# Kernel optimization log

Measured on AMD Instinct MI355X. Metric: run time of the kernel, lower is better.

The kernel has to match this reference:

```python
import jax, jax.numpy as jnp
import numpy as np

CHAN = 128
IN_CHAN = 3
NB_OUT = 10
K = 2  # maxPoolKer


def affine_grid(theta, H, W):
    # theta: [C,2,3] -> grid [C,H,W,2], torch F.affine_grid align_corners=False
    xs = (2.0 * jnp.arange(W, dtype=jnp.float32) + 1.0) / W - 1.0
    ys = (2.0 * jnp.arange(H, dtype=jnp.float32) + 1.0) / H - 1.0
    gx, gy = jnp.meshgrid(xs, ys)  # [H,W]
    base = jnp.stack([gx, gy, jnp.ones_like(gx)], axis=-1)  # [H,W,3]
    return jnp.einsum('crk,hwk->chwr', theta, base)  # [...,0]=x, [...,1]=y


def grid_sample(img, grid):
    # img [M,H,W], grid [M,H,W,2]; bilinear, zeros padding, align_corners=False
    M, H, W = img.shape
    ix = ((grid[..., 0] + 1.0) * W - 1.0) * 0.5
    iy = ((grid[..., 1] + 1.0) * H - 1.0) * 0.5
    x0 = jnp.floor(ix)
    y0 = jnp.floor(iy)
    wx = ix - x0
    wy = iy - y0

    def tap(xi, yi):
        valid = (xi >= 0) & (xi <= W - 1) & (yi >= 0) & (yi <= H - 1)
        xc = jnp.clip(xi, 0, W - 1).astype(jnp.int32)
        yc = jnp.clip(yi, 0, H - 1).astype(jnp.int32)
        v = jax.vmap(lambda im, y, x: im[y, x])(img, yc, xc)
        return jnp.where(valid, v, 0.0)

    v00 = tap(x0, y0)
    v01 = tap(x0 + 1.0, y0)
    v10 = tap(x0, y0 + 1.0)
    v11 = tap(x0 + 1.0, y0 + 1.0)
    return (1.0 - wy) * ((1.0 - wx) * v00 + wx * v01) + wy * ((1.0 - wx) * v10 + wx * v11)


def geom_layer(x, geo, lin, box):
    # x [B,Ci,H,W]; lin [C,Ci]; geo,box [C,2,3]
    B, Ci, H, W = x.shape
    C = lin.shape[0]
    y = jnp.einsum('ci,bihw->bchw', lin, x)  # channel linear combine
    grid = affine_grid(geo, H, W)            # [C,H,W,2], shared across batch
    samp = jax.vmap(lambda yb: grid_sample(yb, grid))(y)  # [B,C,H,W]
    bgrid = affine_grid(box, H, W)
    boxm = grid_sample(jnp.ones((C, H, W), samp.dtype), bgrid)  # BoxPool mask
    return samp * boxm[None]


def maxpool_g(x, k):
    # MaxPool2d_G: depthwise box-filter conv -> argmax -> gather window from padded x
    B, C, H, W = x.shape
    ch, cw = H // k, W // k
    ker = jnp.ones((1, 1, ch, cw), x.dtype) / (ch + cw)
    xr = x.reshape(B * C, 1, H, W)
    conv = jax.lax.conv_general_dilated(
        xr, ker, (1, 1), [(ch // 2, ch // 2), (cw // 2, cw // 2)])
    conv = conv[:, :, :H, :W].reshape(B, C, H * W)
    argm = jnp.argmax(conv, axis=-1)
    r = argm // H  # original code uses origImgSize[0]; assumes square H==W
    c = argm % W
    padH, padW = H + H // k, W + W // k
    top = padH // 2 - H // 2
    left = padW // 2 - W // 2
    padded = jnp.zeros((B, C, padH, padW), x.dtype).at[:, :, top:top + H, left:left + W].set(x)
    r2 = r + H // (2 * k)
    c2 = c + W // (2 * k)
    ri = r2[..., None] + (jnp.arange(ch) - ch // 2)  # [B,C,ch]
    ci = c2[..., None] + (jnp.arange(cw) - cw // 2)  # [B,C,cw]
    gat = jax.vmap(jax.vmap(lambda p, rr, cc: p[rr[:, None], cc[None, :]]))(padded, ri, ci)
    return gat  # [B,C,ch,cw]


def setup_inputs() -> dict:
    key = jax.random.key(0)
    ks = jax.random.split(key, 12)
    eye = jnp.eye(3, dtype=jnp.float32)[:2]  # [2,3]
    x = jax.random.normal(ks[0], (8, IN_CHAN, 64, 64), dtype=jnp.float32)
    geo0 = eye[None] + 0.1 * jax.random.normal(ks[1], (CHAN, 2, 3), dtype=jnp.float32)
    lin0 = jax.random.uniform(ks[2], (CHAN, IN_CHAN), dtype=jnp.float32)
    box0 = eye[None] + 0.1 * jax.random.normal(ks[3], (CHAN, 2, 3), dtype=jnp.float32)
    geos = eye[None, None] + 0.1 * jax.random.normal(ks[4], (3, CHAN, 2, 3), dtype=jnp.float32)
    lins = jax.random.uniform(ks[5], (3, CHAN, CHAN), dtype=jnp.float32)
    boxes = eye[None, None] + 0.1 * jax.random.normal(ks[6], (3, CHAN, 2, 3), dtype=jnp.float32)
    bound = 1.0 / np.sqrt(CHAN)
    dense_w = jax.random.uniform(ks[7], (NB_OUT, CHAN), dtype=jnp.float32, minval=-bound, maxval=bound)
    dense_b = jax.random.uniform(ks[8], (NB_OUT,), dtype=jnp.float32, minval=-bound, maxval=bound)
    return {"x": x, "geo0": geo0, "lin0": lin0, "box0": box0,
            "geos": geos, "lins": lins, "boxes": boxes,
            "dense_w": dense_w, "dense_b": dense_b}


def reference(x, geo0, lin0, box0, geos, lins, boxes, dense_w, dense_b):
    h = geom_layer(x, geo0, lin0, box0)            # inLay: [8,128,64,64]
    h = geom_layer(h, geos[0], lins[0], boxes[0])  # layer 0
    h = maxpool_g(h, K)                            # layer 1 (maxPoolPos=1): [8,128,32,32]
    h = geom_layer(h, geos[1], lins[1], boxes[1])  # layer 2
    h = geom_layer(h, geos[2], lins[2], boxes[2])  # layer 3
    feat = h
    pooled = feat.mean(axis=-1).mean(axis=-1)      # [B,C]
    out = pooled @ dense_w.T + dense_b             # [B,nbOut]
    return out, feat
```

## Files before the change

kernel.cpp:

```cpp
#include <hip/hip_runtime.h>

#define BB 8
#define CC 128

__global__ __launch_bounds__(256) void inlay_sample_kernel(
    const float* __restrict__ x, const float* __restrict__ lin,
    const float* __restrict__ geo, const float* __restrict__ box,
    const float* __restrict__ db, float* __restrict__ out,
    float* __restrict__ head) {
  const int H = 64, W = 64, HW = 4096;
  __shared__ __align__(16) float cp[64 * 68];
  int bc = blockIdx.x;
  int b = bc & 7;
  int c = bc >> 3;
  int tid = threadIdx.x;
  if (bc == 0 && tid < 80) head[tid] = db[tid % 10];
  const float* xb = x + (size_t)b * 3 * HW;

  float w0 = lin[c * 3 + 0], w1 = lin[c * 3 + 1], w2 = lin[c * 3 + 2];

#pragma unroll
  for (int k = 0; k < 4; ++k) {
    int i4 = tid + k * 256;
    int base = i4 * 4;
    float4 f0 = *reinterpret_cast<const float4*>(&xb[base]);
    float4 f1 = *reinterpret_cast<const float4*>(&xb[HW + base]);
    float4 f2 = *reinterpret_cast<const float4*>(&xb[2 * HW + base]);
    float4 cv;
    cv.x = w0 * f0.x + w1 * f1.x + w2 * f2.x;
    cv.y = w0 * f0.y + w1 * f1.y + w2 * f2.y;
    cv.z = w0 * f0.z + w1 * f1.z + w2 * f2.z;
    cv.w = w0 * f0.w + w1 * f1.w + w2 * f2.w;
    int h = i4 >> 4, w = (i4 & 15) * 4;
    *reinterpret_cast<float4*>(&cp[h * 68 + w]) = cv;
  }
  __syncthreads();

  const float* g = geo + c * 6;
  const float* bx = box + c * 6;
  float g0 = g[0], g1 = g[1], g2 = g[2], g3 = g[3], g4 = g[4], g5 = g[5];
  float b0 = bx[0], b1 = bx[1], b2 = bx[2], b3 = bx[3], b4 = bx[4], b5 = bx[5];
  float* o = out + ((size_t)b * CC + c) * HW;

#pragma unroll
  for (int k = 0; k < 16; ++k) {
    int px = tid + k * 256;
    int h = px >> 6, w = px & 63;
    float xs = (2.0f * w + 1.0f) / W - 1.0f;
    float ys = (2.0f * h + 1.0f) / H - 1.0f;
    float gx = g0 * xs + g1 * ys + g2;
    float gy = g3 * xs + g4 * ys + g5;
    float ix = ((gx + 1.0f) * W - 1.0f) * 0.5f;
    float iy = ((gy + 1.0f) * H - 1.0f) * 0.5f;
    float x0 = floorf(ix), y0 = floorf(iy);
    float wx = ix - x0, wy = iy - y0;
    float v[2][2];
#pragma unroll
    for (int dy = 0; dy < 2; ++dy)
#pragma unroll
      for (int dx = 0; dx < 2; ++dx) {
        float xf = x0 + dx, yf = y0 + dy;
        bool valid = (xf >= 0.0f) && (xf <= 63.0f) && (yf >= 0.0f) && (yf <= 63.0f);
        int xi = (int)fminf(fmaxf(xf, 0.0f), 63.0f);
        int yi = (int)fminf(fmaxf(yf, 0.0f), 63.0f);
        v[dy][dx] = valid ? cp[yi * 68 + xi] : 0.0f;
      }
    float samp = (1.0f - wy) * ((1.0f - wx) * v[0][0] + wx * v[0][1]) +
                 wy * ((1.0f - wx) * v[1][0] + wx * v[1][1]);

    float bgx = b0 * xs + b1 * ys + b2;
    float bgy = b3 * xs + b4 * ys + b5;
    float bix = ((bgx + 1.0f) * W - 1.0f) * 0.5f;
    float biy = ((bgy + 1.0f) * H - 1.0f) * 0.5f;
    float bx0 = floorf(bix), by0 = floorf(biy);
    float bwx = bix - bx0, bwy = biy - by0;
    float m[2][2];
#pragma unroll
    for (int dy = 0; dy < 2; ++dy)
#pragma unroll
      for (int dx = 0; dx < 2; ++dx) {
        float xf = bx0 + dx, yf = by0 + dy;
        m[dy][dx] = ((xf >= 0.0f) && (xf <= 63.0f) && (yf >= 0.0f) && (yf <= 63.0f)) ? 1.0f : 0.0f;
      }
    float mask = (1.0f - bwy) * ((1.0f - bwx) * m[0][0] + bwx * m[0][1]) +
                 bwy * ((1.0f - bwx) * m[1][0] + bwx * m[1][1]);
    o[px] = samp * mask;
  }
}

__global__ __launch_bounds__(256) void gemm64_kernel(
    const float* __restrict__ lin, const float* __restrict__ x,
    float* __restrict__ y, int HW) {
  const int Ci = 128;
  __shared__ __align__(16) float As[16][68];
  __shared__ __align__(16) float Bs[16][64];
  int bx = blockIdx.x;
  int b = bx & 7;
  int t = bx >> 3;
  int row0 = (t & 1) * 64;
  int col0 = (t >> 1) * 64;
  const float* xb = x + (size_t)b * Ci * HW;
  float* yb = y + (size_t)b * CC * HW;
  int tid = threadIdx.x;
  int tx = tid & 15, ty = tid >> 4;
  int m = tid >> 2, kq = (tid & 3) * 4;
  int kk = tid >> 4, n4 = (tid & 15) * 4;
  float acc[4][4] = {};
  float4 ra = *reinterpret_cast<const float4*>(&lin[(row0 + m) * Ci + kq]);
  float4 rb = *reinterpret_cast<const float4*>(&xb[(size_t)kk * HW + col0 + n4]);
  for (int k0 = 0; k0 < 128; k0 += 16) {
    __syncthreads();
    As[kq + 0][m] = ra.x; As[kq + 1][m] = ra.y; As[kq + 2][m] = ra.z; As[kq + 3][m] = ra.w;
    *reinterpret_cast<float4*>(&Bs[kk][n4]) = rb;
    __syncthreads();
    if (k0 + 16 < 128) {
      ra = *reinterpret_cast<const float4*>(&lin[(row0 + m) * Ci + k0 + 16 + kq]);
      rb = *reinterpret_cast<const float4*>(&xb[(size_t)(k0 + 16 + kk) * HW + col0 + n4]);
    }
#pragma unroll
    for (int kki = 0; kki < 16; ++kki) {
      float4 a4 = *reinterpret_cast<const float4*>(&As[kki][ty * 4]);
      float4 b4 = *reinterpret_cast<const float4*>(&Bs[kki][tx * 4]);
      float a[4] = {a4.x, a4.y, a4.z, a4.w};
      float bv[4] = {b4.x, b4.y, b4.z, b4.w};
#pragma unroll
      for (int i = 0; i < 4; i++)
#pragma unroll
        for (int j = 0; j < 4; j++) acc[i][j] += a[i] * bv[j];
    }
  }
#pragma unroll
  for (int i = 0; i < 4; i++) {
    float* yr = yb + (size_t)(row0 + ty * 4 + i) * HW + col0 + tx * 4;
    *reinterpret_cast<float4*>(yr) = make_float4(acc[i][0], acc[i][1], acc[i][2], acc[i][3]);
  }
}

__global__ __launch_bounds__(1024, 4) void sampmax_kernel(
    const float* __restrict__ y, const float* __restrict__ geo,
    const float* __restrict__ box, float* __restrict__ out) {
  __shared__ __align__(16) float sp[64 * 68];
  __shared__ __align__(16) float arena[64 * 100];
  __shared__ float wv[16];
  __shared__ int wi[16];
  __shared__ int am_s;
  float* pl = arena;
  float* cb = arena;

  int bc = blockIdx.x;
  int b = bc & 7;
  int c = bc >> 3;
  int tid = threadIdx.x;

  const float* plane = y + ((size_t)b * CC + c) * 4096;
  *reinterpret_cast<float4*>(&pl[tid * 4]) = *reinterpret_cast<const float4*>(&plane[tid * 4]);
  __syncthreads();

  {
    const float* g = geo + c * 6;
    const float* bx = box + c * 6;
    float g0 = g[0], g1 = g[1], g2 = g[2], g3 = g[3], g4 = g[4], g5 = g[5];
    float b0 = bx[0], b1 = bx[1], b2 = bx[2], b3 = bx[3], b4 = bx[4], b5 = bx[5];
#pragma unroll
    for (int k = 0; k < 4; ++k) {
      int px = tid + k * 1024;
      int h = px >> 6, w = px & 63;
      float xs = (2.0f * w + 1.0f) / 64.0f - 1.0f;
      float ys = (2.0f * h + 1.0f) / 64.0f - 1.0f;
      float gx = g0 * xs + g1 * ys + g2;
      float gy = g3 * xs + g4 * ys + g5;
      float ix = ((gx + 1.0f) * 64.0f - 1.0f) * 0.5f;
      float iy = ((gy + 1.0f) * 64.0f - 1.0f) * 0.5f;
      float x0 = floorf(ix), y0 = floorf(iy);
      float wx = ix - x0, wy = iy - y0;
      float v[2][2];
#pragma unroll
      for (int dy = 0; dy < 2; ++dy)
#pragma unroll
        for (int dx = 0; dx < 2; ++dx) {
          float xf = x0 + dx, yf = y0 + dy;
          bool valid = (xf >= 0.0f) && (xf <= 63.0f) && (yf >= 0.0f) && (yf <= 63.0f);
          int xi = (int)fminf(fmaxf(xf, 0.0f), 63.0f);
          int yi = (int)fminf(fmaxf(yf, 0.0f), 63.0f);
          v[dy][dx] = valid ? pl[yi * 64 + xi] : 0.0f;
        }
      float samp = (1.0f - wy) * ((1.0f - wx) * v[0][0] + wx * v[0][1]) +
                   wy * ((1.0f - wx) * v[1][0] + wx * v[1][1]);
      float bgx = b0 * xs + b1 * ys + b2;
      float bgy = b3 * xs + b4 * ys + b5;
      float bix = ((bgx + 1.0f) * 64.0f - 1.0f) * 0.5f;
      float biy = ((bgy + 1.0f) * 64.0f - 1.0f) * 0.5f;
      float bx0 = floorf(bix), by0 = floorf(biy);
      float bwx = bix - bx0, bwy = biy - by0;
      float m[2][2];
#pragma unroll
      for (int dy = 0; dy < 2; ++dy)
#pragma unroll
        for (int dx = 0; dx < 2; ++dx) {
          float xf = bx0 + dx, yf = by0 + dy;
          m[dy][dx] = ((xf >= 0.0f) && (xf <= 63.0f) && (yf >= 0.0f) && (yf <= 63.0f)) ? 1.0f : 0.0f;
        }
      float mask = (1.0f - bwy) * ((1.0f - bwx) * m[0][0] + bwx * m[0][1]) +
                   bwy * ((1.0f - bwx) * m[1][0] + bwx * m[1][1]);
      sp[h * 68 + w] = samp * mask;
    }
  }
  __syncthreads();

  if (tid < 256) {
    int strip = tid >> 4, w4 = (tid & 15) * 4;
    int h0 = strip * 4;
    float4 a = make_float4(0.f, 0.f, 0.f, 0.f);
    float4 keep0 = a, keep1 = a, keep2 = a;
#pragma unroll
    for (int j = 0; j < 32; ++j) {
      int r = h0 + j - 16;
      bool valid = (r >= 0) && (r < 64);
      int rc = valid ? r : 0;
      float4 f = *reinterpret_cast<const float4*>(&sp[rc * 68 + w4]);
      f.x = valid ? f.x : 0.0f; f.y = valid ? f.y : 0.0f;
      f.z = valid ? f.z : 0.0f; f.w = valid ? f.w : 0.0f;
      if (j == 0) keep0 = f;
      if (j == 1) keep1 = f;
      if (j == 2) keep2 = f;
      a.x += f.x; a.y += f.y; a.z += f.z; a.w += f.w;
    }
    *reinterpret_cast<float4*>(&cb[(h0 + 0) * 100 + 16 + w4]) = a;
#pragma unroll
    for (int j = 32; j < 35; ++j) {
      int r = h0 + j - 16;
      bool valid = (r < 64);
      int rc = valid ? r : 0;
      float4 f = *reinterpret_cast<const float4*>(&sp[rc * 68 + w4]);
      f.x = valid ? f.x : 0.0f; f.y = valid ? f.y : 0.0f;
      f.z = valid ? f.z : 0.0f; f.w = valid ? f.w : 0.0f;
      float4 kp = (j == 32) ? keep0 : ((j == 33) ? keep1 : keep2);
      a.x += f.x - kp.x; a.y += f.y - kp.y; a.z += f.z - kp.z; a.w += f.w - kp.w;
      *reinterpret_cast<float4*>(&cb[(h0 + j - 31) * 100 + 16 + w4]) = a;
    }
  } else if (tid < 768) {
    int l = tid - 256;
    int row = l >> 3, gq = l & 7;
    int base = row * 100 + ((gq < 4) ? gq * 4 : 80 + (gq - 4) * 4);
    *reinterpret_cast<float4*>(&cb[base]) = make_float4(0.f, 0.f, 0.f, 0.f);
  }
  __syncthreads();

  float best = -3.402823466e+38f;
  int bidx = 0x7fffffff;
  {
    int h = tid >> 4, w4 = (tid & 15) * 4;
    float s0 = 0.f, k0 = 0.f, k1 = 0.f, k2 = 0.f;
#pragma unroll
    for (int q = 0; q < 8; ++q) {
      float4 f = *reinterpret_cast<const float4*>(&cb[h * 100 + w4 + 4 * q]);
      if (q == 0) { k0 = f.x; k1 = f.y; k2 = f.z; }
      s0 += f.x; s0 += f.y; s0 += f.z; s0 += f.w;
    }
    float4 ft = *reinterpret_cast<const float4*>(&cb[h * 100 + w4 + 32]);
    float s1 = s0 - k0 + ft.x;
    float s2 = s1 - k1 + ft.y;
    float s3 = s2 - k2 + ft.z;
    float sv[4] = {s0, s1, s2, s3};
#pragma unroll
    for (int d = 0; d < 4; ++d) {
      int i = (h << 6) + w4 + d;
      if (sv[d] > best) { best = sv[d]; bidx = i; }
    }
  }
#pragma unroll
  for (int off = 32; off > 0; off >>= 1) {
    float v2 = __shfl_down(best, off);
    int i2 = __shfl_down(bidx, off);
    if (v2 > best || (v2 == best && i2 < bidx)) { best = v2; bidx = i2; }
  }
  if ((tid & 63) == 0) { wv[tid >> 6] = best; wi[tid >> 6] = bidx; }
  __syncthreads();
  if (tid == 0) {
    float bv = wv[0]; int bi = wi[0];
#pragma unroll
    for (int k = 1; k < 16; ++k)
      if (wv[k] > bv || (wv[k] == bv && wi[k] < bi)) { bv = wv[k]; bi = wi[k]; }
    am_s = bi;
  }
  __syncthreads();

  int am = am_s;
  int r = am >> 6, cx = am & 63;
  float* o = out + ((size_t)b * CC + c) * 1024;
  {
    int oi = tid >> 5, oj = tid & 31;
    int rr = r + oi - 16, cj = cx + oj - 16;
    bool v = (rr >= 0) && (rr < 64) && (cj >= 0) && (cj < 64);
    int rrc = v ? rr : 0, cjc = v ? cj : 0;
    o[tid] = v ? sp[rrc * 68 + cjc] : 0.0f;
  }
}

template <bool POOL>
__global__ __launch_bounds__(512) void fused32_kernel(
    const float* __restrict__ lin, const float* __restrict__ x,
    const float* __restrict__ geo, const float* __restrict__ box,
    float* __restrict__ out, const float* __restrict__ dw,
    float* __restrict__ head) {
  const int H = 32, W = 32, HW = 1024;
  __shared__ __align__(16) float pls[4][1024];
  __shared__ float wred[32];
  __shared__ float wsum[4];
  int b = blockIdx.x & 7;
  int c0 = (blockIdx.x >> 3) * 4;
  int tid = threadIdx.x;
  const float* xb = x + (size_t)b * 128 * HW;
  const float* l0 = lin + (c0 + 0) * 128;
  const float* l1 = lin + (c0 + 1) * 128;
  const float* l2 = lin + (c0 + 2) * 128;
  const float* l3 = lin + (c0 + 3) * 128;
  int px2 = tid * 2;

  float2 a0 = make_float2(0.f, 0.f), a1 = a0, a2 = a0, a3 = a0;
#pragma unroll 8
  for (int k = 0; k < 128; ++k) {
    float2 xv = *reinterpret_cast<const float2*>(&xb[(size_t)k * HW + px2]);
    float s0 = l0[k], s1 = l1[k], s2 = l2[k], s3 = l3[k];
    a0.x += s0 * xv.x; a0.y += s0 * xv.y;
    a1.x += s1 * xv.x; a1.y += s1 * xv.y;
    a2.x += s2 * xv.x; a2.y += s2 * xv.y;
    a3.x += s3 * xv.x; a3.y += s3 * xv.y;
  }
  *reinterpret_cast<float2*>(&pls[0][px2]) = a0;
  *reinterpret_cast<float2*>(&pls[1][px2]) = a1;
  *reinterpret_cast<float2*>(&pls[2][px2]) = a2;
  *reinterpret_cast<float2*>(&pls[3][px2]) = a3;
  __syncthreads();

  float psum[4] = {0.f, 0.f, 0.f, 0.f};
#pragma unroll
  for (int c = 0; c < 4; ++c) {
    const float* g = geo + (c0 + c) * 6;
    const float* bxp = box + (c0 + c) * 6;
    float g0 = g[0], g1 = g[1], g2 = g[2], g3 = g[3], g4 = g[4], g5 = g[5];
    float b0 = bxp[0], b1 = bxp[1], b2 = bxp[2], b3 = bxp[3], b4 = bxp[4], b5 = bxp[5];
    float* o = out + ((size_t)b * CC + c0 + c) * HW;
    const float* pl = pls[c];
#pragma unroll
    for (int k = 0; k < 2; ++k) {
      int px = tid + k * 512;
      int h = px >> 5, w = px & 31;
      float xs = (2.0f * w + 1.0f) / W - 1.0f;
      float ys = (2.0f * h + 1.0f) / H - 1.0f;
      float gx = g0 * xs + g1 * ys + g2;
      float gy = g3 * xs + g4 * ys + g5;
      float ix = ((gx + 1.0f) * W - 1.0f) * 0.5f;
      float iy = ((gy + 1.0f) * H - 1.0f) * 0.5f;
      float x0 = floorf(ix), y0 = floorf(iy);
      float wx = ix - x0, wy = iy - y0;
      float v[2][2];
#pragma unroll
      for (int dy = 0; dy < 2; ++dy)
#pragma unroll
        for (int dx = 0; dx < 2; ++dx) {
          float xf = x0 + dx, yf = y0 + dy;
          bool valid = (xf >= 0.0f) && (xf <= 31.0f) && (yf >= 0.0f) && (yf <= 31.0f);
          int xi = (int)fminf(fmaxf(xf, 0.0f), 31.0f);
          int yi = (int)fminf(fmaxf(yf, 0.0f), 31.0f);
          v[dy][dx] = valid ? pl[yi * 32 + xi] : 0.0f;
        }
      float samp = (1.0f - wy) * ((1.0f - wx) * v[0][0] + wx * v[0][1]) +
                   wy * ((1.0f - wx) * v[1][0] + wx * v[1][1]);
      float bgx = b0 * xs + b1 * ys + b2;
      float bgy = b3 * xs + b4 * ys + b5;
      float bix = ((bgx + 1.0f) * W - 1.0f) * 0.5f;
      float biy = ((bgy + 1.0f) * H - 1.0f) * 0.5f;
      float bx0 = floorf(bix), by0 = floorf(biy);
      float bwx = bix - bx0, bwy = biy - by0;
      float m[2][2];
#pragma unroll
      for (int dy = 0; dy < 2; ++dy)
#pragma unroll
        for (int dx = 0; dx < 2; ++dx) {
          float xf = bx0 + dx, yf = by0 + dy;
          m[dy][dx] = ((xf >= 0.0f) && (xf <= 31.0f) && (yf >= 0.0f) && (yf <= 31.0f)) ? 1.0f : 0.0f;
        }
      float mask = (1.0f - bwy) * ((1.0f - bwx) * m[0][0] + bwx * m[0][1]) +
                   bwy * ((1.0f - bwx) * m[1][0] + bwx * m[1][1]);
      float res = samp * mask;
      o[px] = res;
      if (POOL) psum[c] += res;
    }
  }
  if (POOL) {
    int lane = tid & 63, wid = tid >> 6;
#pragma unroll
    for (int c = 0; c < 4; ++c) {
      float r = psum[c];
#pragma unroll
      for (int off = 32; off > 0; off >>= 1) r += __shfl_down(r, off);
      if (lane == 0) wred[c * 8 + wid] = r;
    }
    __syncthreads();
    if (tid < 4) {
      float t = 0.f;
#pragma unroll
      for (int w = 0; w < 8; ++w) t += wred[tid * 8 + w];
      wsum[tid] = t * (1.0f / 1024.0f);
    }
    __syncthreads();
    if (tid < 10) {
      float s = 0.f;
#pragma unroll
      for (int c = 0; c < 4; ++c) s += wsum[c] * dw[tid * 128 + c0 + c];
      atomicAdd(&head[b * 10 + tid], s);
    }
  }
}

extern "C" void kernel_launch(void* const* d_in, const int* in_sizes, int n_in,
                              void* d_out, int out_size, void* d_ws, size_t ws_size,
                              hipStream_t stream) {
  const float* x     = (const float*)d_in[0];
  const float* geo0  = (const float*)d_in[1];
  const float* lin0  = (const float*)d_in[2];
  const float* box0  = (const float*)d_in[3];
  const float* geos  = (const float*)d_in[4];
  const float* lins  = (const float*)d_in[5];
  const float* boxes = (const float*)d_in[6];
  const float* dw    = (const float*)d_in[7];
  const float* db    = (const float*)d_in[8];

  float* out  = (float*)d_out;
  float* feat = out + 80;
  float* ws   = (float*)d_ws;
  float* ws0  = ws;
  float* ws1  = ws + 4194304;

  inlay_sample_kernel<<<dim3(BB * CC), 256, 0, stream>>>(x, lin0, geo0, box0, db, ws1, out);
  gemm64_kernel<<<dim3(1024), 256, 0, stream>>>(lins, ws1, ws0, 4096);
  sampmax_kernel<<<dim3(BB * CC), 1024, 0, stream>>>(ws0, geos, boxes, ws1);
  fused32_kernel<false><<<dim3(256), 512, 0, stream>>>(lins + 16384, ws1, geos + 768, boxes + 768, ws0, nullptr, nullptr);
  fused32_kernel<true><<<dim3(256), 512, 0, stream>>>(lins + 32768, ws0, geos + 1536, boxes + 1536, feat, dw, out);
}
```

Measured before the change: 167.9 us.

## Use zero-padded shared planes for branchless bilinear sampling and reshape block mappings

Shared-memory planes gain a one-element zero border, so bilinear sampling clamps the coordinates once and reads four taps with no per-tap validity checks. The box mask is computed separably in closed form. Block-to-(batch,channel) mapping is changed to channel-fastest, the GEMM moves to a 3D grid, and fused32 handles 2 channels per 256-thread block so twice as many blocks launch. The padded stores become scalar instead of float4, and the extra border initialisation adds a little work.

```diff
diff --git a/kernel.cpp b/kernel.cpp
--- a/kernel.cpp
+++ b/kernel.cpp
@@ -2,6 +2,29 @@
 
 #define BB 8
 #define CC 128
+
+__device__ __forceinline__ float sample_pad(const float* __restrict__ pl, int stride,
+                                            float WF, float ix, float iy) {
+  ix = fminf(fmaxf(ix, -1.0f), WF);
+  iy = fminf(fmaxf(iy, -1.0f), WF);
+  float x0f = floorf(ix), y0f = floorf(iy);
+  float wx = ix - x0f, wy = iy - y0f;
+  int xi = (int)x0f + 1, yi = (int)y0f + 1;
+  const float* p0 = pl + yi * stride + xi;
+  float v00 = p0[0], v01 = p0[1], v10 = p0[stride], v11 = p0[stride + 1];
+  return (1.0f - wy) * ((1.0f - wx) * v00 + wx * v01) +
+         wy * ((1.0f - wx) * v10 + wx * v11);
+}
+
+__device__ __forceinline__ float box_mask(float bix, float biy, float WM1) {
+  float bx0 = floorf(bix), by0 = floorf(biy);
+  float bwx = bix - bx0, bwy = biy - by0;
+  float mx = (((bx0 >= 0.0f) && (bx0 <= WM1)) ? (1.0f - bwx) : 0.0f) +
+             (((bx0 >= -1.0f) && (bx0 <= WM1 - 1.0f)) ? bwx : 0.0f);
+  float my = (((by0 >= 0.0f) && (by0 <= WM1)) ? (1.0f - bwy) : 0.0f) +
+             (((by0 >= -1.0f) && (by0 <= WM1 - 1.0f)) ? bwy : 0.0f);
+  return mx * my;
+}
 
 __global__ __launch_bounds__(256) void inlay_sample_kernel(
     const float* __restrict__ x, const float* __restrict__ lin,
@@ -9,15 +32,22 @@
     const float* __restrict__ db, float* __restrict__ out,
     float* __restrict__ head) {
   const int H = 64, W = 64, HW = 4096;
-  __shared__ __align__(16) float cp[64 * 68];
+  __shared__ float cp[67 * 68];
   int bc = blockIdx.x;
-  int b = bc & 7;
-  int c = bc >> 3;
+  int c = bc & (CC - 1);
+  int b = bc >> 7;
   int tid = threadIdx.x;
   if (bc == 0 && tid < 80) head[tid] = db[tid % 10];
   const float* xb = x + (size_t)b * 3 * HW;
 
   float w0 = lin[c * 3 + 0], w1 = lin[c * 3 + 1], w2 = lin[c * 3 + 2];
+
+  if (tid < 68) {
+    cp[tid] = 0.0f; cp[65 * 68 + tid] = 0.0f; cp[66 * 68 + tid] = 0.0f;
+  } else if (tid < 132) {
+    int r = tid - 67;
+    cp[r * 68 + 0] = 0.0f; cp[r * 68 + 65] = 0.0f; cp[r * 68 + 66] = 0.0f;
+  }
 
 #pragma unroll
   for (int k = 0; k < 4; ++k) {
@@ -26,13 +56,12 @@
     float4 f0 = *reinterpret_cast<const float4*>(&xb[base]);
     float4 f1 = *reinterpret_cast<const float4*>(&xb[HW + base]);
     float4 f2 = *reinterpret_cast<const float4*>(&xb[2 * HW + base]);
-    float4 cv;
-    cv.x = w0 * f0.x + w1 * f1.x + w2 * f2.x;
-    cv.y = w0 * f0.y + w1 * f1.y + w2 * f2.y;
-    cv.z = w0 * f0.z + w1 * f1.z + w2 * f2.z;
-    cv.w = w0 * f0.w + w1 * f1.w + w2 * f2.w;
     int h = i4 >> 4, w = (i4 & 15) * 4;
-    *reinterpret_cast<float4*>(&cp[h * 68 + w]) = cv;
+    float* d = &cp[(h + 1) * 68 + w + 1];
+    d[0] = w0 * f0.x + w1 * f1.x + w2 * f2.x;
+    d[1] = w0 * f0.y + w1 * f1.y + w2 * f2.y;
+    d[2] = w0 * f0.z + w1 * f1.z + w2 * f2.z;
+    d[3] = w0 * f0.w + w1 * f1.w + w2 * f2.w;
   }
   __syncthreads();
 
@@ -48,43 +77,12 @@
     int h = px >> 6, w = px & 63;
     float xs = (2.0f * w + 1.0f) / W - 1.0f;
     float ys = (2.0f * h + 1.0f) / H - 1.0f;
-    float gx = g0 * xs + g1 * ys + g2;
-    float gy = g3 * xs + g4 * ys + g5;
-    float ix = ((gx + 1.0f) * W - 1.0f) * 0.5f;
-    float iy = ((gy + 1.0f) * H - 1.0f) * 0.5f;
-    float x0 = floorf(ix), y0 = floorf(iy);
-    float wx = ix - x0, wy = iy - y0;
-    float v[2][2];
-#pragma unroll
-    for (int dy = 0; dy < 2; ++dy)
-#pragma unroll
-      for (int dx = 0; dx < 2; ++dx) {
-        float xf = x0 + dx, yf = y0 + dy;
-        bool valid = (xf >= 0.0f) && (xf <= 63.0f) && (yf >= 0.0f) && (yf <= 63.0f);
-        int xi = (int)fminf(fmaxf(xf, 0.0f), 63.0f);
-        int yi = (int)fminf(fmaxf(yf, 0.0f), 63.0f);
-        v[dy][dx] = valid ? cp[yi * 68 + xi] : 0.0f;
-      }
-    float samp = (1.0f - wy) * ((1.0f - wx) * v[0][0] + wx * v[0][1]) +
-                 wy * ((1.0f - wx) * v[1][0] + wx * v[1][1]);
-
-    float bgx = b0 * xs + b1 * ys + b2;
-    float bgy = b3 * xs + b4 * ys + b5;
-    float bix = ((bgx + 1.0f) * W - 1.0f) * 0.5f;
-    float biy = ((bgy + 1.0f) * H - 1.0f) * 0.5f;
-    float bx0 = floorf(bix), by0 = floorf(biy);
-    float bwx = bix - bx0, bwy = biy - by0;
-    float m[2][2];
-#pragma unroll
-    for (int dy = 0; dy < 2; ++dy)
-#pragma unroll
-      for (int dx = 0; dx < 2; ++dx) {
-        float xf = bx0 + dx, yf = by0 + dy;
-        m[dy][dx] = ((xf >= 0.0f) && (xf <= 63.0f) && (yf >= 0.0f) && (yf <= 63.0f)) ? 1.0f : 0.0f;
-      }
-    float mask = (1.0f - bwy) * ((1.0f - bwx) * m[0][0] + bwx * m[0][1]) +
-                 bwy * ((1.0f - bwx) * m[1][0] + bwx * m[1][1]);
-    o[px] = samp * mask;
+    float ix = ((g0 * xs + g1 * ys + g2 + 1.0f) * W - 1.0f) * 0.5f;
+    float iy = ((g3 * xs + g4 * ys + g5 + 1.0f) * H - 1.0f) * 0.5f;
+    float samp = sample_pad(cp, 68, 64.0f, ix, iy);
+    float bix = ((b0 * xs + b1 * ys + b2 + 1.0f) * W - 1.0f) * 0.5f;
+    float biy = ((b3 * xs + b4 * ys + b5 + 1.0f) * H - 1.0f) * 0.5f;
+    o[px] = samp * box_mask(bix, biy, 63.0f);
   }
 }
 
@@ -94,15 +92,13 @@
   const int Ci = 128;
   __shared__ __align__(16) float As[16][68];
   __shared__ __align__(16) float Bs[16][64];
-  int bx = blockIdx.x;
-  int b = bx & 7;
-  int t = bx >> 3;
-  int row0 = (t & 1) * 64;
-  int col0 = (t >> 1) * 64;
+  int b = blockIdx.z;
   const float* xb = x + (size_t)b * Ci * HW;
   float* yb = y + (size_t)b * CC * HW;
   int tid = threadIdx.x;
   int tx = tid & 15, ty = tid >> 4;
+  int row0 = blockIdx.y * 64;
+  int col0 = blockIdx.x * 64;
   int m = tid >> 2, kq = (tid & 3) * 4;
   int kk = tid >> 4, n4 = (tid & 15) * 4;
   float acc[4][4] = {};
@@ -148,12 +144,22 @@
   float* cb = arena;
 
   int bc = blockIdx.x;
-  int b = bc & 7;
-  int c = bc >> 3;
+  int c = bc & (CC - 1);
   int tid = threadIdx.x;
 
-  const float* plane = y + ((size_t)b * CC + c) * 4096;
-  *reinterpret_cast<float4*>(&pl[tid * 4]) = *reinterpret_cast<const float4*>(&plane[tid * 4]);
+  if (tid < 68) {
+    pl[tid] = 0.0f; pl[65 * 68 + tid] = 0.0f; pl[66 * 68 + tid] = 0.0f;
+  } else if (tid < 132) {
+    int r = tid - 67;
+    pl[r * 68 + 0] = 0.0f; pl[r * 68 + 65] = 0.0f; pl[r * 68 + 66] = 0.0f;
+  }
+  {
+    const float* plane = y + (size_t)bc * 4096;
+    float4 f = *reinterpret_cast<const float4*>(&plane[tid * 4]);
+    int h = tid >> 4, w = (tid & 15) * 4;
+    float* d = &pl[(h + 1) * 68 + w + 1];
+    d[0] = f.x; d[1] = f.y; d[2] = f.z; d[3] = f.w;
+  }
   __syncthreads();
 
   {
@@ -167,42 +173,12 @@
       int h = px >> 6, w = px & 63;
       float xs = (2.0f * w + 1.0f) / 64.0f - 1.0f;
       float ys = (2.0f * h + 1.0f) / 64.0f - 1.0f;
-      float gx = g0 * xs + g1 * ys + g2;
-      float gy = g3 * xs + g4 * ys + g5;
-      float ix = ((gx + 1.0f) * 64.0f - 1.0f) * 0.5f;
-      float iy = ((gy + 1.0f) * 64.0f - 1.0f) * 0.5f;
-      float x0 = floorf(ix), y0 = floorf(iy);
-      float wx = ix - x0, wy = iy - y0;
-      float v[2][2];
-#pragma unroll
-      for (int dy = 0; dy < 2; ++dy)
-#pragma unroll
-        for (int dx = 0; dx < 2; ++dx) {
-          float xf = x0 + dx, yf = y0 + dy;
-          bool valid = (xf >= 0.0f) && (xf <= 63.0f) && (yf >= 0.0f) && (yf <= 63.0f);
-          int xi = (int)fminf(fmaxf(xf, 0.0f), 63.0f);
-          int yi = (int)fminf(fmaxf(yf, 0.0f), 63.0f);
-          v[dy][dx] = valid ? pl[yi * 64 + xi] : 0.0f;
-        }
-      float samp = (1.0f - wy) * ((1.0f - wx) * v[0][0] + wx * v[0][1]) +
-                   wy * ((1.0f - wx) * v[1][0] + wx * v[1][1]);
-      float bgx = b0 * xs + b1 * ys + b2;
-      float bgy = b3 * xs + b4 * ys + b5;
-      float bix = ((bgx + 1.0f) * 64.0f - 1.0f) * 0.5f;
-      float biy = ((bgy + 1.0f) * 64.0f - 1.0f) * 0.5f;
-      float bx0 = floorf(bix), by0 = floorf(biy);
-      float bwx = bix - bx0, bwy = biy - by0;
-      float m[2][2];
-#pragma unroll
-      for (int dy = 0; dy < 2; ++dy)
-#pragma unroll
-        for (int dx = 0; dx < 2; ++dx) {
-          float xf = bx0 + dx, yf = by0 + dy;
-          m[dy][dx] = ((xf >= 0.0f) && (xf <= 63.0f) && (yf >= 0.0f) && (yf <= 63.0f)) ? 1.0f : 0.0f;
-        }
-      float mask = (1.0f - bwy) * ((1.0f - bwx) * m[0][0] + bwx * m[0][1]) +
-                   bwy * ((1.0f - bwx) * m[1][0] + bwx * m[1][1]);
-      sp[h * 68 + w] = samp * mask;
+      float ix = ((g0 * xs + g1 * ys + g2 + 1.0f) * 64.0f - 1.0f) * 0.5f;
+      float iy = ((g3 * xs + g4 * ys + g5 + 1.0f) * 64.0f - 1.0f) * 0.5f;
+      float samp = sample_pad(pl, 68, 64.0f, ix, iy);
+      float bix = ((b0 * xs + b1 * ys + b2 + 1.0f) * 64.0f - 1.0f) * 0.5f;
+      float biy = ((b3 * xs + b4 * ys + b5 + 1.0f) * 64.0f - 1.0f) * 0.5f;
+      sp[h * 68 + w] = samp * box_mask(bix, biy, 63.0f);
     }
   }
   __syncthreads();
@@ -287,7 +263,7 @@
 
   int am = am_s;
   int r = am >> 6, cx = am & 63;
-  float* o = out + ((size_t)b * CC + c) * 1024;
+  float* o = out + (size_t)bc * 1024;
   {
     int oi = tid >> 5, oj = tid & 31;
     int rr = r + oi - 16, cj = cx + oj - 16;
@@ -298,44 +274,62 @@
 }
 
 template <bool POOL>
-__global__ __launch_bounds__(512) void fused32_kernel(
+__global__ __launch_bounds__(256) void fused32_kernel(
     const float* __restrict__ lin, const float* __restrict__ x,
     const float* __restrict__ geo, const float* __restrict__ box,
     float* __restrict__ out, const float* __restrict__ dw,
     float* __restrict__ head) {
   const int H = 32, W = 32, HW = 1024;
-  __shared__ __align__(16) float pls[4][1024];
-  __shared__ float wred[32];
-  __shared__ float wsum[4];
+  __shared__ float pls[2][35 * 36];
+  __shared__ float wred[8];
+  __shared__ float wsum[2];
   int b = blockIdx.x & 7;
-  int c0 = (blockIdx.x >> 3) * 4;
+  int c0 = (blockIdx.x >> 3) * 2;
   int tid = threadIdx.x;
   const float* xb = x + (size_t)b * 128 * HW;
   const float* l0 = lin + (c0 + 0) * 128;
   const float* l1 = lin + (c0 + 1) * 128;
-  const float* l2 = lin + (c0 + 2) * 128;
-  const float* l3 = lin + (c0 + 3) * 128;
-  int px2 = tid * 2;
-
-  float2 a0 = make_float2(0.f, 0.f), a1 = a0, a2 = a0, a3 = a0;
+  int px4 = tid * 4;
+
+  if (tid < 36) {
+#pragma unroll
+    for (int cch = 0; cch < 2; ++cch) {
+      pls[cch][tid] = 0.0f;
+      pls[cch][33 * 36 + tid] = 0.0f;
+      pls[cch][34 * 36 + tid] = 0.0f;
+    }
+  } else if (tid < 68) {
+    int r = tid - 35;
+#pragma unroll
+    for (int cch = 0; cch < 2; ++cch) {
+      pls[cch][r * 36 + 0] = 0.0f;
+      pls[cch][r * 36 + 33] = 0.0f;
+      pls[cch][r * 36 + 34] = 0.0f;
+      pls[cch][r * 36 + 35] = 0.0f;
+    }
+  }
+
+  float4 acc0 = make_float4(0.f, 0.f, 0.f, 0.f);
+  float4 acc1 = acc0;
 #pragma unroll 8
   for (int k = 0; k < 128; ++k) {
-    float2 xv = *reinterpret_cast<const float2*>(&xb[(size_t)k * HW + px2]);
-    float s0 = l0[k], s1 = l1[k], s2 = l2[k], s3 = l3[k];
-    a0.x += s0 * xv.x; a0.y += s0 * xv.y;
-    a1.x += s1 * xv.x; a1.y += s1 * xv.y;
-    a2.x += s2 * xv.x; a2.y += s2 * xv.y;
-    a3.x += s3 * xv.x; a3.y += s3 * xv.y;
-  }
-  *reinterpret_cast<float2*>(&pls[0][px2]) = a0;
-  *reinterpret_cast<float2*>(&pls[1][px2]) = a1;
-  *reinterpret_cast<float2*>(&pls[2][px2]) = a2;
-  *reinterpret_cast<float2*>(&pls[3][px2]) = a3;
-  __syncthreads();
-
-  float psum[4] = {0.f, 0.f, 0.f, 0.f};
-#pragma unroll
-  for (int c = 0; c < 4; ++c) {
+    float4 xv = *reinterpret_cast<const float4*>(&xb[(size_t)k * HW + px4]);
+    float s0 = l0[k], s1 = l1[k];
+    acc0.x += s0 * xv.x; acc0.y += s0 * xv.y; acc0.z += s0 * xv.z; acc0.w += s0 * xv.w;
+    acc1.x += s1 * xv.x; acc1.y += s1 * xv.y; acc1.z += s1 * xv.z; acc1.w += s1 * xv.w;
+  }
+  {
+    int h = px4 >> 5, w = px4 & 31;
+    float* d0 = &pls[0][(h + 1) * 36 + w + 1];
+    d0[0] = acc0.x; d0[1] = acc0.y; d0[2] = acc0.z; d0[3] = acc0.w;
+    float* d1 = &pls[1][(h + 1) * 36 + w + 1];
+    d1[0] = acc1.x; d1[1] = acc1.y; d1[2] = acc1.z; d1[3] = acc1.w;
+  }
+  __syncthreads();
+
+  float psum[2] = {0.f, 0.f};
+#pragma unroll
+  for (int c = 0; c < 2; ++c) {
     const float* g = geo + (c0 + c) * 6;
     const float* bxp = box + (c0 + c) * 6;
     float g0 = g[0], g1 = g[1], g2 = g[2], g3 = g[3], g4 = g[4], g5 = g[5];
@@ -343,47 +337,17 @@
     float* o = out + ((size_t)b * CC + c0 + c) * HW;
     const float* pl = pls[c];
 #pragma unroll
-    for (int k = 0; k < 2; ++k) {
-      int px = tid + k * 512;
+    for (int k = 0; k < 4; ++k) {
+      int px = tid + k * 256;
       int h = px >> 5, w = px & 31;
       float xs = (2.0f * w + 1.0f) / W - 1.0f;
       float ys = (2.0f * h + 1.0f) / H - 1.0f;
-      float gx = g0 * xs + g1 * ys + g2;
-      float gy = g3 * xs + g4 * ys + g5;
-      float ix = ((gx + 1.0f) * W - 1.0f) * 0.5f;
-      float iy = ((gy + 1.0f) * H - 1.0f) * 0.5f;
-      float x0 = floorf(ix), y0 = floorf(iy);
-      float wx = ix - x0, wy = iy - y0;
-      float v[2][2];
-#pragma unroll
-      for (int dy = 0; dy < 2; ++dy)
-#pragma unroll
-        for (int dx = 0; dx < 2; ++dx) {
-          float xf = x0 + dx, yf = y0 + dy;
-          bool valid = (xf >= 0.0f) && (xf <= 31.0f) && (yf >= 0.0f) && (yf <= 31.0f);
-          int xi = (int)fminf(fmaxf(xf, 0.0f), 31.0f);
-          int yi = (int)fminf(fmaxf(yf, 0.0f), 31.0f);
-          v[dy][dx] = valid ? pl[yi * 32 + xi] : 0.0f;
-        }
-      float samp = (1.0f - wy) * ((1.0f - wx) * v[0][0] + wx * v[0][1]) +
-                   wy * ((1.0f - wx) * v[1][0] + wx * v[1][1]);
-      float bgx = b0 * xs + b1 * ys + b2;
-      float bgy = b3 * xs + b4 * ys + b5;
-      float bix = ((bgx + 1.0f) * W - 1.0f) * 0.5f;
-      float biy = ((bgy + 1.0f) * H - 1.0f) * 0.5f;
-      float bx0 = floorf(bix), by0 = floorf(biy);
-      float bwx = bix - bx0, bwy = biy - by0;
-      float m[2][2];
-#pragma unroll
-      for (int dy = 0; dy < 2; ++dy)
-#pragma unroll
-        for (int dx = 0; dx < 2; ++dx) {
-          float xf = bx0 + dx, yf = by0 + dy;
-          m[dy][dx] = ((xf >= 0.0f) && (xf <= 31.0f) && (yf >= 0.0f) && (yf <= 31.0f)) ? 1.0f : 0.0f;
-        }
-      float mask = (1.0f - bwy) * ((1.0f - bwx) * m[0][0] + bwx * m[0][1]) +
-                   bwy * ((1.0f - bwx) * m[1][0] + bwx * m[1][1]);
-      float res = samp * mask;
+      float ix = ((g0 * xs + g1 * ys + g2 + 1.0f) * W - 1.0f) * 0.5f;
+      float iy = ((g3 * xs + g4 * ys + g5 + 1.0f) * H - 1.0f) * 0.5f;
+      float samp = sample_pad(pl, 36, 32.0f, ix, iy);
+      float bix = ((b0 * xs + b1 * ys + b2 + 1.0f) * W - 1.0f) * 0.5f;
+      float biy = ((b3 * xs + b4 * ys + b5 + 1.0f) * H - 1.0f) * 0.5f;
+      float res = samp * box_mask(bix, biy, 31.0f);
       o[px] = res;
       if (POOL) psum[c] += res;
     }
@@ -391,24 +355,20 @@
   if (POOL) {
     int lane = tid & 63, wid = tid >> 6;
 #pragma unroll
-    for (int c = 0; c < 4; ++c) {
+    for (int c = 0; c < 2; ++c) {
       float r = psum[c];
 #pragma unroll
       for (int off = 32; off > 0; off >>= 1) r += __shfl_down(r, off);
-      if (lane == 0) wred[c * 8 + wid] = r;
+      if (lane == 0) wred[c * 4 + wid] = r;
     }
     __syncthreads();
-    if (tid < 4) {
-      float t = 0.f;
-#pragma unroll
-      for (int w = 0; w < 8; ++w) t += wred[tid * 8 + w];
+    if (tid < 2) {
+      float t = wred[tid * 4] + wred[tid * 4 + 1] + wred[tid * 4 + 2] + wred[tid * 4 + 3];
       wsum[tid] = t * (1.0f / 1024.0f);
     }
     __syncthreads();
     if (tid < 10) {
-      float s = 0.f;
-#pragma unroll
-      for (int c = 0; c < 4; ++c) s += wsum[c] * dw[tid * 128 + c0 + c];
+      float s = wsum[0] * dw[tid * 128 + c0] + wsum[1] * dw[tid * 128 + c0 + 1];
       atomicAdd(&head[b * 10 + tid], s);
     }
   }
@@ -434,8 +394,8 @@
   float* ws1  = ws + 4194304;
 
   inlay_sample_kernel<<<dim3(BB * CC), 256, 0, stream>>>(x, lin0, geo0, box0, db, ws1, out);
-  gemm64_kernel<<<dim3(1024), 256, 0, stream>>>(lins, ws1, ws0, 4096);
+  gemm64_kernel<<<dim3(64, 2, BB), 256, 0, stream>>>(lins, ws1, ws0, 4096);
   sampmax_kernel<<<dim3(BB * CC), 1024, 0, stream>>>(ws0, geos, boxes, ws1);
-  fused32_kernel<false><<<dim3(256), 512, 0, stream>>>(lins + 16384, ws1, geos + 768, boxes + 768, ws0, nullptr, nullptr);
-  fused32_kernel<true><<<dim3(256), 512, 0, stream>>>(lins + 32768, ws0, geos + 1536, boxes + 1536, feat, dw, out);
-}
+  fused32_kernel<false><<<dim3(512), 256, 0, stream>>>(lins + 16384, ws1, geos + 768, boxes + 768, ws0, nullptr, nullptr);
+  fused32_kernel<true><<<dim3(512), 256, 0, stream>>>(lins + 32768, ws0, geos + 1536, boxes + 1536, feat, dw, out);
+}
```

Result: faster. 157.5 us (-6.2%).
